# Performance work log

Measured on AMD Instinct MI355X. Metric: run time of the kernel, lower is better.

The kernel has to match this reference:

```python
import jax, jax.numpy as jnp
import numpy as np

N, E, F_IN, H, T, OUT, ATTR = 20000, 640000, 128, 128, 12, 64, 4


def _glorot(key, shape):
    lim = 1.0 / np.sqrt(shape[0])
    return jax.random.uniform(key, shape, jnp.float32, -lim, lim)


def setup_inputs() -> dict:
    key = jax.random.key(0)
    ks = jax.random.split(key, 48)
    inp = {
        "x": jax.random.normal(ks[0], (N, F_IN, T), jnp.float32),
        "edge_attr": jax.random.uniform(ks[1], (E, ATTR), jnp.float32),
        "edge_index": jax.random.randint(ks[2], (2, E), 0, N, jnp.int32),
    }
    k = 3
    for i, cin in enumerate([F_IN, H]):
        gi = cin + 2 * H
        inp[f"gw{i}"] = _glorot(ks[k], (cin, H)); k += 1
        inp[f"gb{i}"] = jnp.zeros((H,), jnp.float32)
        for g in ["f", "i", "o", "c"]:
            inp[f"w{g}{i}"] = _glorot(ks[k], (gi, H)); k += 1
            inp[f"b{g}{i}"] = jnp.zeros((H,), jnp.float32)
    inp["ow"] = _glorot(ks[k], (H, OUT)); k += 1
    inp["ob"] = jnp.zeros((OUT,), jnp.float32)
    return inp


def _forward(edge_index, x, edge_attr, gw0, gb0, wf0, bf0, wi0, bi0, wo0, bo0, wc0, bc0,
             gw1, gb1, wf1, bf1, wi1, bi1, wo1, bo1, wc1, bc1, ow, ob):
    n = x.shape[0]
    ew = edge_attr[:, -1]
    row, col = edge_index[0], edge_index[1]
    # GCN normalization with self-loops (PyG gcn_norm, improved=False)
    sl = jnp.arange(n, dtype=row.dtype)
    r = jnp.concatenate([row, sl])
    c = jnp.concatenate([col, sl])
    w = jnp.concatenate([ew, jnp.ones((n,), ew.dtype)])
    deg = jax.ops.segment_sum(w, c, num_segments=n)
    dis = jnp.where(deg > 0, 1.0, 0.0) * jax.lax.rsqrt(jnp.where(deg > 0, deg, 1.0))
    norm = dis[r] * w * dis[c]  # [E+N]

    params = [(gw0, gb0, wf0, bf0, wi0, bi0, wo0, bo0, wc0, bc0),
              (gw1, gb1, wf1, bf1, wi1, bi1, wo1, bo1, wc1, bc1)]

    def gcn(xt, gw, gb):
        xw = xt @ gw  # [N,H]
        return jax.ops.segment_sum(norm[:, None] * xw[r], c, num_segments=n) + gb

    def cell(xt, h, cc, p):
        gw, gb, wf, bf, wi, bi, wo, bo, wc, bc = p
        g = jax.nn.sigmoid(gcn(xt, gw, gb))
        zu = jnp.concatenate([xt, g, h], axis=-1)  # [N, in+2H]
        f_t = jax.nn.sigmoid(zu @ wf + bf)
        i_t = jax.nn.sigmoid(zu @ wi + bi)
        o_t = jax.nn.sigmoid(zu @ wo + bo)
        c_t = jnp.tanh(zu @ wc + bc)
        cn = f_t * cc + i_t * c_t
        hn = o_t * jnp.tanh(cn)
        return hn, cn

    z = jnp.zeros((n, H), x.dtype)

    def step(carry, xt):
        inp_t = xt
        new = []
        for i2, p in enumerate(params):
            h, cc = cell(inp_t, carry[i2][0], carry[i2][1], p)
            new.append((h, cc))
            inp_t = h
        return tuple(new), None

    xs = jnp.transpose(x, (2, 0, 1))  # [T, N, F]
    carry, _ = jax.lax.scan(step, tuple((z, z) for _ in params), xs)
    return carry[-1][0] @ ow + ob  # output_activation = Identity


def reference(x, edge_attr, edge_index, gw0, gb0, wf0, bf0, wi0, bi0, wo0, bo0, wc0, bc0,
              gw1, gb1, wf1, bf1, wi1, bi1, wo1, bo1, wc1, bc1, ow, ob):
    return _forward(edge_index, x, edge_attr, gw0, gb0, wf0, bf0, wi0, bi0, wo0, bo0, wc0, bc0,
                    gw1, gb1, wf1, bf1, wi1, bi1, wo1, bo1, wc1, bc1, ow, ob)
```

## Files before the change

kernel.cpp:

```cpp
#include <hip/hip_runtime.h>
#include <hip/hip_bf16.h>

typedef unsigned short u16;
typedef unsigned int   u32;
typedef __attribute__((ext_vector_type(8))) short bf16x8;
typedef __attribute__((ext_vector_type(4))) float f32x4;

#define HDIM 128
#define TSTEPS 12
#define OUTD 64
#define NTMAJ 1536
#define NTB   3072

#define AS1 __attribute__((address_space(1)))
#define AS3 __attribute__((address_space(3)))

struct u32x3 { u32 x, y, z; };

__device__ __forceinline__ void glds16(const void* g, void* l) {
  __builtin_amdgcn_global_load_lds((const AS1 u32*)g, (AS3 u32*)l, 16, 0, 0);
}

__device__ __forceinline__ float bflo(u32 u) { return __uint_as_float(u << 16); }
__device__ __forceinline__ float bfhi(u32 u) { return __uint_as_float(u & 0xffff0000u); }
__device__ __forceinline__ u16 f2bf(float x) {
  union { float f; u32 u; } v; v.f = x;
  return (u16)((v.u + 0x7fffu + ((v.u >> 16) & 1u)) >> 16);
}
__device__ __forceinline__ float sigm(float x) { return 1.0f / (1.0f + __expf(-x)); }
__device__ __forceinline__ float tanh_f(float x) { return 1.0f - 2.0f / (__expf(2.0f * x) + 1.0f); }


__global__ void k_init(int* cnt, int* cursor, int N) {
  int i = blockIdx.x * 256 + threadIdx.x;
  if (i < N) { cnt[i] = 1; cursor[i] = 0; }
}

__global__ void k_zero(u32* p, int n) {
  int i = blockIdx.x * 256 + threadIdx.x;
  if (i < n) p[i] = 0;
}

__global__ void k_xpose(const float* __restrict__ x, u16* __restrict__ xb, int N) {
  int i = blockIdx.x * 256 + threadIdx.x;
  if (i >= N * HDIM) return;
  const float* src = x + (size_t)i * 12;
  float4 a = *(const float4*)src;
  float4 b = *(const float4*)(src + 4);
  float4 c = *(const float4*)(src + 8);
  float v[12] = { a.x,a.y,a.z,a.w,b.x,b.y,b.z,b.w,c.x,c.y,c.z,c.w };
#pragma unroll
  for (int t = 0; t < 12; ++t) xb[(size_t)t * N * HDIM + i] = f2bf(v[t]);
}

__global__ void k_cnt(const int* __restrict__ ei, int* cnt, int E) {
  int e = blockIdx.x * 256 + threadIdx.x;
  if (e >= E) return;
  atomicAdd(&cnt[ei[E + e]], 1);
}

__global__ void k_scan(const int* __restrict__ cnt, int* __restrict__ rp, int n) {
  __shared__ int sums[1024];
  int tid = threadIdx.x;
  int chunk = (n + 1023) / 1024;
  int start = tid * chunk;
  int end = start + chunk; if (end > n) end = n;
  int s = 0;
  for (int i = start; i < end; ++i) s += cnt[i];
  sums[tid] = s;
  __syncthreads();
  for (int off = 1; off < 1024; off <<= 1) {
    int v = (tid >= off) ? sums[tid - off] : 0;
    __syncthreads();
    sums[tid] += v;
    __syncthreads();
  }
  int run = (tid == 0) ? 0 : sums[tid - 1];
  for (int i = start; i < end; ++i) { rp[i] = run; run += cnt[i]; }
  if (tid == 1023) rp[n] = sums[1023];
}

__global__ void k_scatter(const int* __restrict__ ei, const float* __restrict__ ea,
                          const int* __restrict__ rp, int* cursor, uint2* ee, int E) {
  int e = blockIdx.x * 256 + threadIdx.x;
  if (e >= E) return;
  int row = ei[e], col = ei[E + e];
  int pos = atomicAdd(&cursor[col], 1);
  int idx = rp[col] + 1 + pos;
  ee[idx] = make_uint2((u32)row * NTB, __float_as_uint(ea[e * 4 + 3]));
}

__global__ void k_degcsr(const int* __restrict__ rp, uint2* ee, float* dis, int N) {
  int j = blockIdx.x;
  int lane = threadIdx.x;
  int beg = rp[j], end = rp[j + 1];
  float s = 0.f;
  for (int i = beg + 1 + lane; i < end; i += 64) s += __uint_as_float(ee[i].y);
#pragma unroll
  for (int o = 32; o; o >>= 1) s += __shfl_down(s, o);
  if (lane == 0) {
    dis[j] = rsqrtf(1.0f + s);
    ee[beg] = make_uint2((u32)j * NTB, __float_as_uint(1.0f));
  }
}

__global__ void k_enrm(const int* __restrict__ rp, const float* __restrict__ dis,
                       uint2* ee, int N) {
  int j = blockIdx.x;
  int lane = threadIdx.x;
  int beg = rp[j], end = rp[j + 1];
  float dj = dis[j];
  for (int i = beg + lane; i < end; i += 64) {
    uint2 q = ee[i];
    ee[i].y = __float_as_uint(dis[q.x / NTB] * __uint_as_float(q.y) * dj);
  }
}

__global__ void k_wt(const float* __restrict__ src, u16* __restrict__ dst, int K, int J, int ldK) {
  int idx = blockIdx.x * 256 + threadIdx.x;
  if (idx >= K * J) return;
  int k = idx / J, j = idx % J;
  dst[j * ldK + k] = f2bf(src[idx]);
}

__global__ void k_wt4(const float* wf, const float* wi, const float* wo, const float* wc,
                      u16* __restrict__ dst) {
  int idx = blockIdx.x * 256 + threadIdx.x;
  if (idx >= 512 * 384) return;
  int p = idx / 384, k = idx % 384;
  int g = (p >> 4) & 3;
  int hc = (p & 15) | ((p >> 6) << 4);
  const float* w[4] = { wf, wi, wo, wc };
  dst[p * 384 + k] = f2bf(w[g][k * HDIM + hc]);
}

__global__ void k_bias4(const float* bf, const float* bi, const float* bo, const float* bc,
                        float* dst) {
  int p = blockIdx.x * 256 + threadIdx.x;
  if (p >= 512) return;
  int g = (p >> 4) & 3;
  int hc = (p & 15) | ((p >> 6) << 4);
  const float* b[4] = { bf, bi, bo, bc };
  dst[p] = b[g][hc];
}

__global__ __launch_bounds__(256)
void k_gcnlin(const u16* __restrict__ A, const u16* __restrict__ wt,
              u16* __restrict__ out, int N, int nh) {
  __shared__ u16 lA[128 * 32];
  __shared__ u16 lB[128 * 32];
  const int t = blockIdx.y;
  const int tid = threadIdx.x;
  const int row0 = blockIdx.x * 128;
  const int wave = tid >> 6, lane = tid & 63;
  const int wm = (wave >> 1) * 64, wn = (wave & 1) * 64;
  const int fr = lane & 15, fk = (lane >> 4) * 8;
  const int lr = tid >> 2, lc = (tid & 3) * 8;
  u16* ldA = lA + wave * 512;
  u16* ldB = lB + wave * 512;
  const u16* ga1 = A + (size_t)t * nh + (size_t)(row0 + lr) * HDIM + lc;
  const u16* ga2 = ga1 + (size_t)64 * HDIM;
  const u16* gb1 = wt + (size_t)lr * HDIM + lc;
  const u16* gb2 = gb1 + (size_t)64 * HDIM;

  f32x4 acc[4][4] = {};
  for (int k0 = 0; k0 < 128; k0 += 32) {
    glds16(ga1 + k0, ldA);
    glds16(ga2 + k0, ldA + 2048);
    glds16(gb1 + k0, ldB);
    glds16(gb2 + k0, ldB + 2048);
    __syncthreads();
    bf16x8 af[4], bfx[4];
#pragma unroll
    for (int m = 0; m < 4; ++m) af[m]  = *(const bf16x8*)&lA[(wm + m * 16 + fr) * 32 + fk];
#pragma unroll
    for (int n = 0; n < 4; ++n) bfx[n] = *(const bf16x8*)&lB[(wn + n * 16 + fr) * 32 + fk];
#pragma unroll
    for (int m = 0; m < 4; ++m)
#pragma unroll
      for (int n = 0; n < 4; ++n)
        acc[m][n] = __builtin_amdgcn_mfma_f32_16x16x32_bf16(af[m], bfx[n], acc[m][n], 0, 0, 0);
    __syncthreads();
  }
  const int fq4 = (lane >> 4) * 4;
#pragma unroll
  for (int m = 0; m < 4; ++m)
#pragma unroll
    for (int n = 0; n < 4; ++n) {
      const int colg = wn + n * 16 + fr;
#pragma unroll
      for (int i = 0; i < 4; ++i) {
        const int rowg = row0 + wm + m * 16 + fq4 + i;
        if (rowg < N) out[(size_t)rowg * NTMAJ + t * HDIM + colg] = f2bf(acc[m][n][i]);
      }
    }
}

__global__ __launch_bounds__(256)
void k_gate3(const u16* __restrict__ p0, u32 st0,
             const u16* __restrict__ p1, u32 st1,
             const u16* __restrict__ p2, u32 st2,
             const u16* __restrict__ wt, const float* __restrict__ b4p,
             float* __restrict__ cst, u16* __restrict__ hout, int M) {
  __shared__ u16 lA[128 * 32];
  __shared__ u16 lB[128 * 32];
  const int col0 = blockIdx.y * 128;
  const int tid = threadIdx.x;
  const int row0 = blockIdx.x * 128;
  const int wave = tid >> 6, lane = tid & 63;
  const int wm = (wave >> 1) * 64, wn = (wave & 1) * 64;
  const int fr = lane & 15, fk = (lane >> 4) * 8;
  const int lr = tid >> 2, lc = (tid & 3) * 8;
  u16* ldA = lA + wave * 512;
  u16* ldB = lB + wave * 512;
  const u16* a1[3]; const u16* a2[3];
  a1[0] = p0 + (size_t)(row0 + lr) * st0 + lc;  a2[0] = a1[0] + (size_t)64 * st0;
  a1[1] = p1 + (size_t)(row0 + lr) * st1 + lc;  a2[1] = a1[1] + (size_t)64 * st1;
  a1[2] = p2 + (size_t)(row0 + lr) * st2 + lc;  a2[2] = a1[2] + (size_t)64 * st2;
  const u16* gb1 = wt + (size_t)(col0 + lr) * 384 + lc;
  const u16* gb2 = gb1 + (size_t)64 * 384;

  f32x4 acc[4][4] = {};
#pragma unroll
  for (int ks = 0; ks < 12; ++ks) {
    const int seg = ks >> 2;
    const int kk = (ks & 3) * 32;
    glds16(a1[seg] + kk, ldA);
    glds16(a2[seg] + kk, ldA + 2048);
    glds16(gb1 + ks * 32, ldB);
    glds16(gb2 + ks * 32, ldB + 2048);
    __syncthreads();
    bf16x8 af[4], bfx[4];
#pragma unroll
    for (int m = 0; m < 4; ++m) af[m]  = *(const bf16x8*)&lA[(wm + m * 16 + fr) * 32 + fk];
#pragma unroll
    for (int n = 0; n < 4; ++n) bfx[n] = *(const bf16x8*)&lB[(wn + n * 16 + fr) * 32 + fk];
#pragma unroll
    for (int m = 0; m < 4; ++m)
#pragma unroll
      for (int n = 0; n < 4; ++n)
        acc[m][n] = __builtin_amdgcn_mfma_f32_16x16x32_bf16(af[m], bfx[n], acc[m][n], 0, 0, 0);
    __syncthreads();
  }

  const int fq4 = (lane >> 4) * 4;
  const int hc = fr | ((blockIdx.y * 2 + (wave & 1)) << 4);
  const int colbase = col0 + wn + fr;
  const float bb0 = b4p[colbase];
  const float bb1 = b4p[colbase + 16];
  const float bb2 = b4p[colbase + 32];
  const float bb3 = b4p[colbase + 48];
#pragma unroll
  for (int m = 0; m < 4; ++m)
#pragma unroll
    for (int i = 0; i < 4; ++i) {
      const int rowg = row0 + wm + m * 16 + fq4 + i;
      if (rowg < M) {
        float f_ = sigm(acc[m][0][i] + bb0);
        float i_ = sigm(acc[m][1][i] + bb1);
        float o_ = sigm(acc[m][2][i] + bb2);
        float cd = tanh_f(acc[m][3][i] + bb3);
        size_t idx = (size_t)rowg * HDIM + hc;
        float cn = f_ * cst[idx] + i_ * cd;
        cst[idx] = cn;
        hout[idx] = f2bf(o_ * tanh_f(cn));
      }
    }
}

__global__ void k_aggB(const u16* __restrict__ xw, const int* __restrict__ rp,
                       const uint2* __restrict__ ee, const float* __restrict__ gbias,
                       u16* __restrict__ g, int N) {
  __shared__ uint2 s_e[256];
  __shared__ float s_b[128];
  const int j = blockIdx.x;
  const int tid = threadIdx.x;
  if (tid < 128) s_b[tid] = gbias[tid];
  const int beg = rp[j], end = rp[j + 1];
  const char* base = (const char*)xw;
  const u32 myoff = (u32)tid * 12;
  float a0 = 0.f, a1 = 0.f, a2 = 0.f, a3 = 0.f, a4 = 0.f, a5 = 0.f;
  for (int cb = beg; cb < end; cb += 256) {
    int mc = end - cb; if (mc > 256) mc = 256;
    if (tid < mc) s_e[tid] = ee[cb + tid];
    __syncthreads();
    for (int e = 0; e < mc; ++e) {
      uint2 r = s_e[e];
      float w = __uint_as_float(r.y);
      u32x3 v = *(const u32x3*)(base + (r.x + myoff));
      a0 += w * bflo(v.x); a1 += w * bfhi(v.x);
      a2 += w * bflo(v.y); a3 += w * bfhi(v.y);
      a4 += w * bflo(v.z); a5 += w * bfhi(v.z);
    }
    __syncthreads();
  }
  const int e0 = tid * 6;
  float r0 = sigm(a0 + s_b[e0 & 127]);
  float r1 = sigm(a1 + s_b[(e0 + 1) & 127]);
  float r2 = sigm(a2 + s_b[(e0 + 2) & 127]);
  float r3 = sigm(a3 + s_b[(e0 + 3) & 127]);
  float r4 = sigm(a4 + s_b[(e0 + 4) & 127]);
  float r5 = sigm(a5 + s_b[(e0 + 5) & 127]);
  u32x3 o;
  o.x = ((u32)f2bf(r1) << 16) | (u32)f2bf(r0);
  o.y = ((u32)f2bf(r3) << 16) | (u32)f2bf(r2);
  o.z = ((u32)f2bf(r5) << 16) | (u32)f2bf(r4);
  *(u32x3*)((char*)g + ((size_t)j * NTB + myoff)) = o;
}

__global__ void k_out(const u16* __restrict__ h, const float* __restrict__ ow,
                      const float* __restrict__ ob, float* __restrict__ out, int M) {
  __shared__ float lw[HDIM * OUTD];
  __shared__ float lb[OUTD];
  int tid = threadIdx.x;
  for (int i = tid; i < HDIM * OUTD; i += 256) lw[i] = ow[i];
  if (tid < OUTD) lb[tid] = ob[tid];
  __syncthreads();
  int j = tid & 63;
  int nl = tid >> 6;
  int n = blockIdx.x * 4 + nl;
  if (n >= M) return;
  const u16* hr = h + (size_t)n * HDIM;
  float s = lb[j];
#pragma unroll 4
  for (int k = 0; k < HDIM; ++k) s += __uint_as_float(((u32)hr[k]) << 16) * lw[k * OUTD + j];
  out[(size_t)n * OUTD + j] = s;
}

extern "C" void kernel_launch(void* const* d_in, const int* in_sizes, int n_in,
                              void* d_out, int out_size, void* d_ws, size_t ws_size,
                              hipStream_t stream) {
  const float* x  = (const float*)d_in[0];
  const float* ea = (const float*)d_in[1];
  const int*   ei = (const int*)d_in[2];
  const float* gw[2] = { (const float*)d_in[3],  (const float*)d_in[13] };
  const float* gb[2] = { (const float*)d_in[4],  (const float*)d_in[14] };
  const float* wg[2][4] = {
    { (const float*)d_in[5],  (const float*)d_in[7],  (const float*)d_in[9],  (const float*)d_in[11] },
    { (const float*)d_in[15], (const float*)d_in[17], (const float*)d_in[19], (const float*)d_in[21] } };
  const float* bg[2][4] = {
    { (const float*)d_in[6],  (const float*)d_in[8],  (const float*)d_in[10], (const float*)d_in[12] },
    { (const float*)d_in[16], (const float*)d_in[18], (const float*)d_in[20], (const float*)d_in[22] } };
  const float* ow = (const float*)d_in[23];
  const float* ob = (const float*)d_in[24];
  float* out = (float*)d_out;

  const int N = in_sizes[0] / (HDIM * TSTEPS);
  const int E = in_sizes[2] / 2;
  const int nh = N * HDIM;
  const int tnh = TSTEPS * nh;

  size_t off = 0;
  auto alloc = [&](size_t bytes) -> void* {
    void* p = (char*)d_ws + off;
    off += (bytes + 255) & ~(size_t)255;
    return p;
  };
  u16* xb     = (u16*)alloc((size_t)tnh * 2);
  u16* g_nm   = (u16*)alloc((size_t)tnh * 2);
  u16* h0_all = (u16*)alloc((size_t)(TSTEPS + 1) * nh * 2);
  float* cst  = (float*)alloc((size_t)nh * 4);
  uint2* ee   = (uint2*)alloc((size_t)(E + N) * 8);
  float* dis  = (float*)alloc((size_t)N * 4);
  int* cnt    = (int*)alloc((size_t)N * 4);
  int* cursor = (int*)alloc((size_t)N * 4);
  int* rp     = (int*)alloc((size_t)(N + 1) * 4);
  u16* gwT[2] = { (u16*)alloc(HDIM * HDIM * 2), (u16*)alloc(HDIM * HDIM * 2) };
  u16* w4T[2] = { (u16*)alloc(512 * 384 * 2),   (u16*)alloc(512 * 384 * 2) };
  float* b4[2] = { (float*)alloc(512 * 4), (float*)alloc(512 * 4) };
  alloc(131072);

  u16* XW0 = h0_all;
  u16* XW1 = xb;
  u16* H1[2] = { xb, xb + (size_t)nh };

  k_init<<<(N + 255) / 256, 256, 0, stream>>>(cnt, cursor, N);
  k_xpose<<<(nh + 255) / 256, 256, 0, stream>>>(x, xb, N);
  k_cnt<<<(E + 255) / 256, 256, 0, stream>>>(ei, cnt, E);
  k_scan<<<1, 1024, 0, stream>>>(cnt, rp, N);
  k_scatter<<<(E + 255) / 256, 256, 0, stream>>>(ei, ea, rp, cursor, ee, E);
  k_degcsr<<<N, 64, 0, stream>>>(rp, ee, dis, N);
  k_enrm<<<N, 64, 0, stream>>>(rp, dis, ee, N);
  for (int l = 0; l < 2; ++l) {
    k_wt<<<(HDIM * HDIM + 255) / 256, 256, 0, stream>>>(gw[l], gwT[l], HDIM, HDIM, HDIM);
    k_wt4<<<(512 * 384 + 255) / 256, 256, 0, stream>>>(wg[l][0], wg[l][1], wg[l][2], wg[l][3], w4T[l]);
    k_bias4<<<2, 256, 0, stream>>>(bg[l][0], bg[l][1], bg[l][2], bg[l][3], b4[l]);
  }

  const int nb = (N + 127) / 128;

  k_gcnlin<<<dim3(nb, TSTEPS), 256, 0, stream>>>(xb, gwT[0], XW0, N, nh);
  k_aggB<<<N, 256, 0, stream>>>(XW0, rp, ee, gb[0], g_nm, N);
  k_zero<<<(nh / 2 + 255) / 256, 256, 0, stream>>>((u32*)h0_all, nh / 2);
  k_zero<<<(nh + 255) / 256, 256, 0, stream>>>((u32*)cst, nh);

  for (int t = 0; t < TSTEPS; ++t)
    k_gate3<<<dim3(nb, 4), 256, 0, stream>>>(
        xb + (size_t)t * nh, HDIM,
        g_nm + (size_t)t * HDIM, NTMAJ,
        h0_all + (size_t)t * nh, HDIM,
        w4T[0], b4[0], cst, h0_all + (size_t)(t + 1) * nh, N);

  k_gcnlin<<<dim3(nb, TSTEPS), 256, 0, stream>>>(h0_all + nh, gwT[1], XW1, N, nh);
  k_aggB<<<N, 256, 0, stream>>>(XW1, rp, ee, gb[1], g_nm, N);
  k_zero<<<(nh / 2 + 255) / 256, 256, 0, stream>>>((u32*)H1[1], nh / 2);
  k_zero<<<(nh + 255) / 256, 256, 0, stream>>>((u32*)cst, nh);

  for (int t = 0; t < TSTEPS; ++t)
    k_gate3<<<dim3(nb, 4), 256, 0, stream>>>(
        h0_all + (size_t)(t + 1) * nh, HDIM,
        g_nm + (size_t)t * HDIM, NTMAJ,
        H1[(t + 1) & 1], HDIM,
        w4T[1], b4[1], cst, H1[t & 1], N);

  k_out<<<(N + 3) / 4, 256, 0, stream>>>(H1[1], ow, ob, out, N);
}
```

Baseline: 1.605 ms.

## Hoist input and GCN gate projections out of recurrence, chunk timesteps

Splits the LSTM gate GEMM into a time-parallel part (x and GCN-output columns, K=256) computed in batched chunks of three timesteps, and a recurrent part (h only, K=128) run per step with 64-row tiles. The intent is to shorten the serial critical path and raise parallelism in the non-recurrent work. The first step uses a special kernel that skips the h GEMM and the zero state, and the zeroing kernels go away. Aggregation is rewritten as a 64-thread per-(node,timestep) kernel over a timestep-major layout, and chunking keeps intermediate buffers small. In exchange, bf16 partial sums must be written and re-read, costing extra memory traffic and a rounding step.

```diff
diff --git a/kernel.cpp b/kernel.cpp
--- a/kernel.cpp
+++ b/kernel.cpp
@@ -9,13 +9,10 @@
 #define HDIM 128
 #define TSTEPS 12
 #define OUTD 64
-#define NTMAJ 1536
-#define NTB   3072
+#define CH_T 3
 
 #define AS1 __attribute__((address_space(1)))
 #define AS3 __attribute__((address_space(3)))
-
-struct u32x3 { u32 x, y, z; };
 
 __device__ __forceinline__ void glds16(const void* g, void* l) {
   __builtin_amdgcn_global_load_lds((const AS1 u32*)g, (AS3 u32*)l, 16, 0, 0);
@@ -34,11 +31,6 @@
 __global__ void k_init(int* cnt, int* cursor, int N) {
   int i = blockIdx.x * 256 + threadIdx.x;
   if (i < N) { cnt[i] = 1; cursor[i] = 0; }
-}
-
-__global__ void k_zero(u32* p, int n) {
-  int i = blockIdx.x * 256 + threadIdx.x;
-  if (i < n) p[i] = 0;
 }
 
 __global__ void k_xpose(const float* __restrict__ x, u16* __restrict__ xb, int N) {
@@ -87,7 +79,7 @@
   int row = ei[e], col = ei[E + e];
   int pos = atomicAdd(&cursor[col], 1);
   int idx = rp[col] + 1 + pos;
-  ee[idx] = make_uint2((u32)row * NTB, __float_as_uint(ea[e * 4 + 3]));
+  ee[idx] = make_uint2((u32)row << 8, __float_as_uint(ea[e * 4 + 3]));
 }
 
 __global__ void k_degcsr(const int* __restrict__ rp, uint2* ee, float* dis, int N) {
@@ -100,7 +92,7 @@
   for (int o = 32; o; o >>= 1) s += __shfl_down(s, o);
   if (lane == 0) {
     dis[j] = rsqrtf(1.0f + s);
-    ee[beg] = make_uint2((u32)j * NTB, __float_as_uint(1.0f));
+    ee[beg] = make_uint2((u32)j << 8, __float_as_uint(1.0f));
   }
 }
 
@@ -112,7 +104,7 @@
   float dj = dis[j];
   for (int i = beg + lane; i < end; i += 64) {
     uint2 q = ee[i];
-    ee[i].y = __float_as_uint(dis[q.x / NTB] * __uint_as_float(q.y) * dj);
+    ee[i].y = __float_as_uint(dis[q.x >> 8] * __uint_as_float(q.y) * dj);
   }
 }
 
@@ -123,15 +115,26 @@
   dst[j * ldK + k] = f2bf(src[idx]);
 }
 
-__global__ void k_wt4(const float* wf, const float* wi, const float* wo, const float* wc,
-                      u16* __restrict__ dst) {
+__global__ void k_wt4r(const float* wf, const float* wi, const float* wo, const float* wc,
+                       u16* __restrict__ dst) {
   int idx = blockIdx.x * 256 + threadIdx.x;
-  if (idx >= 512 * 384) return;
-  int p = idx / 384, k = idx % 384;
+  if (idx >= 512 * 128) return;
+  int p = idx / 128, k = idx % 128;
   int g = (p >> 4) & 3;
   int hc = (p & 15) | ((p >> 6) << 4);
   const float* w[4] = { wf, wi, wo, wc };
-  dst[p * 384 + k] = f2bf(w[g][k * HDIM + hc]);
+  dst[p * 128 + k] = f2bf(w[g][(256 + k) * HDIM + hc]);
+}
+
+__global__ void k_wt4xg(const float* wf, const float* wi, const float* wo, const float* wc,
+                        u16* __restrict__ dst) {
+  int idx = blockIdx.x * 256 + threadIdx.x;
+  if (idx >= 512 * 256) return;
+  int p = idx / 256, k = idx % 256;
+  int g = (p >> 4) & 3;
+  int hc = (p & 15) | ((p >> 6) << 4);
+  const float* w[4] = { wf, wi, wo, wc };
+  dst[p * 256 + k] = f2bf(w[g][k * HDIM + hc]);
 }
 
 __global__ void k_bias4(const float* bf, const float* bi, const float* bo, const float* bc,
@@ -191,19 +194,17 @@
 #pragma unroll
       for (int i = 0; i < 4; ++i) {
         const int rowg = row0 + wm + m * 16 + fq4 + i;
-        if (rowg < N) out[(size_t)rowg * NTMAJ + t * HDIM + colg] = f2bf(acc[m][n][i]);
+        if (rowg < N) out[(size_t)t * nh + (size_t)rowg * HDIM + colg] = f2bf(acc[m][n][i]);
       }
     }
 }
 
 __global__ __launch_bounds__(256)
-void k_gate3(const u16* __restrict__ p0, u32 st0,
-             const u16* __restrict__ p1, u32 st1,
-             const u16* __restrict__ p2, u32 st2,
-             const u16* __restrict__ wt, const float* __restrict__ b4p,
-             float* __restrict__ cst, u16* __restrict__ hout, int M) {
+void k_partial(const u16* __restrict__ segX, const u16* __restrict__ segG,
+               const u16* __restrict__ wxg, u16* __restrict__ outP, int N, int nh) {
   __shared__ u16 lA[128 * 32];
   __shared__ u16 lB[128 * 32];
+  const int tt = blockIdx.z;
   const int col0 = blockIdx.y * 128;
   const int tid = threadIdx.x;
   const int row0 = blockIdx.x * 128;
@@ -213,22 +214,22 @@
   const int lr = tid >> 2, lc = (tid & 3) * 8;
   u16* ldA = lA + wave * 512;
   u16* ldB = lB + wave * 512;
-  const u16* a1[3]; const u16* a2[3];
-  a1[0] = p0 + (size_t)(row0 + lr) * st0 + lc;  a2[0] = a1[0] + (size_t)64 * st0;
-  a1[1] = p1 + (size_t)(row0 + lr) * st1 + lc;  a2[1] = a1[1] + (size_t)64 * st1;
-  a1[2] = p2 + (size_t)(row0 + lr) * st2 + lc;  a2[2] = a1[2] + (size_t)64 * st2;
-  const u16* gb1 = wt + (size_t)(col0 + lr) * 384 + lc;
-  const u16* gb2 = gb1 + (size_t)64 * 384;
+  const u16* aX1 = segX + (size_t)tt * nh + (size_t)(row0 + lr) * HDIM + lc;
+  const u16* aX2 = aX1 + (size_t)64 * HDIM;
+  const u16* aG1 = segG + (size_t)tt * nh + (size_t)(row0 + lr) * HDIM + lc;
+  const u16* aG2 = aG1 + (size_t)64 * HDIM;
+  const u16* b1 = wxg + (size_t)(col0 + lr) * 256 + lc;
+  const u16* b2 = b1 + (size_t)64 * 256;
 
   f32x4 acc[4][4] = {};
 #pragma unroll
-  for (int ks = 0; ks < 12; ++ks) {
-    const int seg = ks >> 2;
-    const int kk = (ks & 3) * 32;
-    glds16(a1[seg] + kk, ldA);
-    glds16(a2[seg] + kk, ldA + 2048);
-    glds16(gb1 + ks * 32, ldB);
-    glds16(gb2 + ks * 32, ldB + 2048);
+  for (int ks = 0; ks < 8; ++ks) {
+    const u16* s1 = (ks < 4) ? (aX1 + ks * 32) : (aG1 + (ks - 4) * 32);
+    const u16* s2 = (ks < 4) ? (aX2 + ks * 32) : (aG2 + (ks - 4) * 32);
+    glds16(s1, ldA);
+    glds16(s2, ldA + 2048);
+    glds16(b1 + ks * 32, ldB);
+    glds16(b2 + ks * 32, ldB + 2048);
     __syncthreads();
     bf16x8 af[4], bfx[4];
 #pragma unroll
@@ -237,6 +238,59 @@
     for (int n = 0; n < 4; ++n) bfx[n] = *(const bf16x8*)&lB[(wn + n * 16 + fr) * 32 + fk];
 #pragma unroll
     for (int m = 0; m < 4; ++m)
+#pragma unroll
+      for (int n = 0; n < 4; ++n)
+        acc[m][n] = __builtin_amdgcn_mfma_f32_16x16x32_bf16(af[m], bfx[n], acc[m][n], 0, 0, 0);
+    __syncthreads();
+  }
+  const int fq4 = (lane >> 4) * 4;
+  u16* outT = outP + (size_t)tt * N * 512;
+#pragma unroll
+  for (int m = 0; m < 4; ++m)
+#pragma unroll
+    for (int n = 0; n < 4; ++n) {
+      const int colg = col0 + wn + n * 16 + fr;
+#pragma unroll
+      for (int i = 0; i < 4; ++i) {
+        const int rowg = row0 + wm + m * 16 + fq4 + i;
+        if (rowg < N) outT[(size_t)rowg * 512 + colg] = f2bf(acc[m][n][i]);
+      }
+    }
+}
+
+__global__ __launch_bounds__(256)
+void k_gate64(const u16* __restrict__ hprev, const u16* __restrict__ wr,
+              const float* __restrict__ b4p, const u16* __restrict__ pp,
+              float* __restrict__ cst, u16* __restrict__ hout, int M) {
+  __shared__ u16 lA[64 * 32];
+  __shared__ u16 lB[128 * 32];
+  const int col0 = blockIdx.y * 128;
+  const int row0 = blockIdx.x * 64;
+  const int tid = threadIdx.x;
+  const int wave = tid >> 6, lane = tid & 63;
+  const int wm = (wave >> 1) * 32, wn = (wave & 1) * 64;
+  const int fr = lane & 15, fk = (lane >> 4) * 8;
+  const int lr = tid >> 2, lc = (tid & 3) * 8;
+  u16* ldA = lA + wave * 512;
+  u16* ldB = lB + wave * 512;
+  const u16* ga  = hprev + (size_t)(row0 + lr) * HDIM + lc;
+  const u16* gb1 = wr + (size_t)(col0 + lr) * HDIM + lc;
+  const u16* gb2 = gb1 + (size_t)64 * HDIM;
+
+  f32x4 acc[2][4] = {};
+#pragma unroll
+  for (int k0 = 0; k0 < 128; k0 += 32) {
+    glds16(ga + k0, ldA);
+    glds16(gb1 + k0, ldB);
+    glds16(gb2 + k0, ldB + 2048);
+    __syncthreads();
+    bf16x8 af[2], bfx[4];
+#pragma unroll
+    for (int m = 0; m < 2; ++m) af[m]  = *(const bf16x8*)&lA[(wm + m * 16 + fr) * 32 + fk];
+#pragma unroll
+    for (int n = 0; n < 4; ++n) bfx[n] = *(const bf16x8*)&lB[(wn + n * 16 + fr) * 32 + fk];
+#pragma unroll
+    for (int m = 0; m < 2; ++m)
 #pragma unroll
       for (int n = 0; n < 4; ++n)
         acc[m][n] = __builtin_amdgcn_mfma_f32_16x16x32_bf16(af[m], bfx[n], acc[m][n], 0, 0, 0);
@@ -251,15 +305,16 @@
   const float bb2 = b4p[colbase + 32];
   const float bb3 = b4p[colbase + 48];
 #pragma unroll
-  for (int m = 0; m < 4; ++m)
+  for (int m = 0; m < 2; ++m)
 #pragma unroll
     for (int i = 0; i < 4; ++i) {
       const int rowg = row0 + wm + m * 16 + fq4 + i;
       if (rowg < M) {
-        float f_ = sigm(acc[m][0][i] + bb0);
-        float i_ = sigm(acc[m][1][i] + bb1);
-        float o_ = sigm(acc[m][2][i] + bb2);
-        float cd = tanh_f(acc[m][3][i] + bb3);
+        const u16* pr = pp + (size_t)rowg * 512 + colbase;
+        float f_ = sigm(acc[m][0][i] + bb0 + bflo(pr[0]));
+        float i_ = sigm(acc[m][1][i] + bb1 + bflo(pr[16]));
+        float o_ = sigm(acc[m][2][i] + bb2 + bflo(pr[32]));
+        float cd = tanh_f(acc[m][3][i] + bb3 + bflo(pr[48]));
         size_t idx = (size_t)rowg * HDIM + hc;
         float cn = f_ * cst[idx] + i_ * cd;
         cst[idx] = cn;
@@ -268,44 +323,66 @@
     }
 }
 
-__global__ void k_aggB(const u16* __restrict__ xw, const int* __restrict__ rp,
-                       const uint2* __restrict__ ee, const float* __restrict__ gbias,
-                       u16* __restrict__ g, int N) {
-  __shared__ uint2 s_e[256];
-  __shared__ float s_b[128];
-  const int j = blockIdx.x;
-  const int tid = threadIdx.x;
-  if (tid < 128) s_b[tid] = gbias[tid];
-  const int beg = rp[j], end = rp[j + 1];
-  const char* base = (const char*)xw;
-  const u32 myoff = (u32)tid * 12;
-  float a0 = 0.f, a1 = 0.f, a2 = 0.f, a3 = 0.f, a4 = 0.f, a5 = 0.f;
-  for (int cb = beg; cb < end; cb += 256) {
-    int mc = end - cb; if (mc > 256) mc = 256;
-    if (tid < mc) s_e[tid] = ee[cb + tid];
-    __syncthreads();
-    for (int e = 0; e < mc; ++e) {
-      uint2 r = s_e[e];
+__global__ void k_cell0(const u16* __restrict__ pp, const float* __restrict__ b4p,
+                        float* __restrict__ cst, u16* __restrict__ hout, int total) {
+  int i = blockIdx.x * 256 + threadIdx.x;
+  if (i >= total) return;
+  int node = i >> 7, hc = i & 127;
+  int p0 = (hc & 15) | ((hc >> 4) << 6);
+  const u16* pr = pp + (size_t)node * 512 + p0;
+  float i_ = sigm(bflo(pr[16]) + b4p[p0 + 16]);
+  float o_ = sigm(bflo(pr[32]) + b4p[p0 + 32]);
+  float cd = tanh_f(bflo(pr[48]) + b4p[p0 + 48]);
+  float cn = i_ * cd;
+  cst[i] = cn;
+  hout[i] = f2bf(o_ * tanh_f(cn));
+}
+
+__global__ void k_agg(const u16* __restrict__ xw, const int* __restrict__ rp,
+                      const uint2* __restrict__ ee, const float* __restrict__ gb,
+                      u16* __restrict__ g, int N) {
+  __shared__ uint2 s_e[64];
+  const char* xwb = (const char*)xw;
+  int bid = blockIdx.x;
+  int j = bid % N;
+  u32 tbase = (u32)(bid - j) << 8;
+  int lane = threadIdx.x;
+  int beg = rp[j], end = rp[j + 1];
+  const int sl = lane & 31, half = lane >> 5;
+  const u32 slB = (u32)sl * 8;
+  float a0 = 0.f, a1 = 0.f, a2 = 0.f, a3 = 0.f;
+  for (int cb = beg; cb < end; cb += 64) {
+    int mc = end - cb; if (mc > 64) mc = 64;
+    uint2 q;
+    if (lane < mc) { q = ee[cb + lane]; q.x += tbase; }
+    else { q.x = tbase; q.y = 0u; }
+    s_e[lane] = q;
+    __syncthreads();
+    int np = (mc + 1) >> 1;
+    for (int p = 0; p < np; ++p) {
+      uint2 r = s_e[p * 2 + half];
       float w = __uint_as_float(r.y);
-      u32x3 v = *(const u32x3*)(base + (r.x + myoff));
-      a0 += w * bflo(v.x); a1 += w * bfhi(v.x);
-      a2 += w * bflo(v.y); a3 += w * bfhi(v.y);
-      a4 += w * bflo(v.z); a5 += w * bfhi(v.z);
+      uint2 v = *(const uint2*)(xwb + (r.x + slB));
+      a0 += w * bflo(v.x);
+      a1 += w * bfhi(v.x);
+      a2 += w * bflo(v.y);
+      a3 += w * bfhi(v.y);
     }
     __syncthreads();
   }
-  const int e0 = tid * 6;
-  float r0 = sigm(a0 + s_b[e0 & 127]);
-  float r1 = sigm(a1 + s_b[(e0 + 1) & 127]);
-  float r2 = sigm(a2 + s_b[(e0 + 2) & 127]);
-  float r3 = sigm(a3 + s_b[(e0 + 3) & 127]);
-  float r4 = sigm(a4 + s_b[(e0 + 4) & 127]);
-  float r5 = sigm(a5 + s_b[(e0 + 5) & 127]);
-  u32x3 o;
-  o.x = ((u32)f2bf(r1) << 16) | (u32)f2bf(r0);
-  o.y = ((u32)f2bf(r3) << 16) | (u32)f2bf(r2);
-  o.z = ((u32)f2bf(r5) << 16) | (u32)f2bf(r4);
-  *(u32x3*)((char*)g + ((size_t)j * NTB + myoff)) = o;
+  a0 += __shfl_xor(a0, 32);
+  a1 += __shfl_xor(a1, 32);
+  a2 += __shfl_xor(a2, 32);
+  a3 += __shfl_xor(a3, 32);
+  if (half == 0) {
+    float4 bv = *(const float4*)(gb + sl * 4);
+    a0 = sigm(a0 + bv.x); a1 = sigm(a1 + bv.y);
+    a2 = sigm(a2 + bv.z); a3 = sigm(a3 + bv.w);
+    uint2 o;
+    o.x = ((u32)f2bf(a1) << 16) | (u32)f2bf(a0);
+    o.y = ((u32)f2bf(a3) << 16) | (u32)f2bf(a2);
+    *(uint2*)((char*)g + (((size_t)bid) << 8) + slB) = o;
+  }
 }
 
 __global__ void k_out(const u16* __restrict__ h, const float* __restrict__ ow,
@@ -357,21 +434,22 @@
     return p;
   };
   u16* xb     = (u16*)alloc((size_t)tnh * 2);
-  u16* g_nm   = (u16*)alloc((size_t)tnh * 2);
-  u16* h0_all = (u16*)alloc((size_t)(TSTEPS + 1) * nh * 2);
+  u16* h0_all = (u16*)alloc((size_t)TSTEPS * nh * 2);
+  u16* XWc    = (u16*)alloc((size_t)CH_T * nh * 2);
+  u16* gc     = (u16*)alloc((size_t)CH_T * nh * 2);
+  u16* Pc     = (u16*)alloc((size_t)CH_T * N * 512 * 2);
   float* cst  = (float*)alloc((size_t)nh * 4);
   uint2* ee   = (uint2*)alloc((size_t)(E + N) * 8);
   float* dis  = (float*)alloc((size_t)N * 4);
   int* cnt    = (int*)alloc((size_t)N * 4);
   int* cursor = (int*)alloc((size_t)N * 4);
   int* rp     = (int*)alloc((size_t)(N + 1) * 4);
-  u16* gwT[2] = { (u16*)alloc(HDIM * HDIM * 2), (u16*)alloc(HDIM * HDIM * 2) };
-  u16* w4T[2] = { (u16*)alloc(512 * 384 * 2),   (u16*)alloc(512 * 384 * 2) };
+  u16* gwT[2]  = { (u16*)alloc(HDIM * HDIM * 2), (u16*)alloc(HDIM * HDIM * 2) };
+  u16* w4r[2]  = { (u16*)alloc(512 * 128 * 2), (u16*)alloc(512 * 128 * 2) };
+  u16* w4xg[2] = { (u16*)alloc(512 * 256 * 2), (u16*)alloc(512 * 256 * 2) };
   float* b4[2] = { (float*)alloc(512 * 4), (float*)alloc(512 * 4) };
   alloc(131072);
 
-  u16* XW0 = h0_all;
-  u16* XW1 = xb;
   u16* H1[2] = { xb, xb + (size_t)nh };
 
   k_init<<<(N + 255) / 256, 256, 0, stream>>>(cnt, cursor, N);
@@ -383,35 +461,34 @@
   k_enrm<<<N, 64, 0, stream>>>(rp, dis, ee, N);
   for (int l = 0; l < 2; ++l) {
     k_wt<<<(HDIM * HDIM + 255) / 256, 256, 0, stream>>>(gw[l], gwT[l], HDIM, HDIM, HDIM);
-    k_wt4<<<(512 * 384 + 255) / 256, 256, 0, stream>>>(wg[l][0], wg[l][1], wg[l][2], wg[l][3], w4T[l]);
+    k_wt4r<<<(512 * 128 + 255) / 256, 256, 0, stream>>>(wg[l][0], wg[l][1], wg[l][2], wg[l][3], w4r[l]);
+    k_wt4xg<<<(512 * 256 + 255) / 256, 256, 0, stream>>>(wg[l][0], wg[l][1], wg[l][2], wg[l][3], w4xg[l]);
     k_bias4<<<2, 256, 0, stream>>>(bg[l][0], bg[l][1], bg[l][2], bg[l][3], b4[l]);
   }
 
   const int nb = (N + 127) / 128;
-
-  k_gcnlin<<<dim3(nb, TSTEPS), 256, 0, stream>>>(xb, gwT[0], XW0, N, nh);
-  k_aggB<<<N, 256, 0, stream>>>(XW0, rp, ee, gb[0], g_nm, N);
-  k_zero<<<(nh / 2 + 255) / 256, 256, 0, stream>>>((u32*)h0_all, nh / 2);
-  k_zero<<<(nh + 255) / 256, 256, 0, stream>>>((u32*)cst, nh);
-
-  for (int t = 0; t < TSTEPS; ++t)
-    k_gate3<<<dim3(nb, 4), 256, 0, stream>>>(
-        xb + (size_t)t * nh, HDIM,
-        g_nm + (size_t)t * HDIM, NTMAJ,
-        h0_all + (size_t)t * nh, HDIM,
-        w4T[0], b4[0], cst, h0_all + (size_t)(t + 1) * nh, N);
-
-  k_gcnlin<<<dim3(nb, TSTEPS), 256, 0, stream>>>(h0_all + nh, gwT[1], XW1, N, nh);
-  k_aggB<<<N, 256, 0, stream>>>(XW1, rp, ee, gb[1], g_nm, N);
-  k_zero<<<(nh / 2 + 255) / 256, 256, 0, stream>>>((u32*)H1[1], nh / 2);
-  k_zero<<<(nh + 255) / 256, 256, 0, stream>>>((u32*)cst, nh);
-
-  for (int t = 0; t < TSTEPS; ++t)
-    k_gate3<<<dim3(nb, 4), 256, 0, stream>>>(
-        h0_all + (size_t)(t + 1) * nh, HDIM,
-        g_nm + (size_t)t * HDIM, NTMAJ,
-        H1[(t + 1) & 1], HDIM,
-        w4T[1], b4[1], cst, H1[t & 1], N);
-
+  const int nb64 = (N + 63) / 64;
+  const int NCH = TSTEPS / CH_T;
+
+  for (int l = 0; l < 2; ++l) {
+    const u16* src = (l == 0) ? xb : h0_all;
+    for (int c = 0; c < NCH; ++c) {
+      const u16* srcC = src + (size_t)c * CH_T * nh;
+      k_gcnlin<<<dim3(nb, CH_T), 256, 0, stream>>>(srcC, gwT[l], XWc, N, nh);
+      k_agg<<<CH_T * N, 64, 0, stream>>>(XWc, rp, ee, gb[l], gc, N);
+      k_partial<<<dim3(nb, 4, CH_T), 256, 0, stream>>>(srcC, gc, w4xg[l], Pc, N, nh);
+      for (int tt = 0; tt < CH_T; ++tt) {
+        const int t = c * CH_T + tt;
+        u16* hdst = (l == 0) ? (h0_all + (size_t)t * nh) : H1[t & 1];
+        const u16* Pt = Pc + (size_t)tt * N * 512;
+        if (t == 0) {
+          k_cell0<<<(nh + 255) / 256, 256, 0, stream>>>(Pt, b4[l], cst, hdst, nh);
+        } else {
+          const u16* hsrc = (l == 0) ? (h0_all + (size_t)(t - 1) * nh) : H1[(t - 1) & 1];
+          k_gate64<<<dim3(nb64, 4), 256, 0, stream>>>(hsrc, w4r[l], b4[l], Pt, cst, hdst, N);
+        }
+      }
+    }
+  }
   k_out<<<(N + 3) / 4, 256, 0, stream>>>(H1[1], ow, ob, out, N);
 }
```

Result: faster. 1.469 ms (-8.4%).
